# Kernel tuning notes

Measured on AMD Instinct MI355X. Metric: run time of the kernel, lower is better.

Reference implementation:

```python
import math
import jax, jax.numpy as jnp
import numpy as np
from jax import lax

# ---- static config (mirrors RPN init + typical torchvision anchor setup) ----
IMG_H = IMG_W = 800
LEVELS = [(200, 200, 4, 32), (100, 100, 8, 64), (50, 50, 16, 128), (25, 25, 32, 256), (13, 13, 64, 512)]  # (h, w, stride, anchor_size)
RATIOS = (0.5, 1.0, 2.0)
COUNTS = tuple(h * w * len(RATIOS) for (h, w, _, _) in LEVELS)  # (120000,30000,7500,1875,507)
A_TOTAL = sum(COUNTS)  # 159882
PRE_NMS = 2000
POST_NMS = 1000
NMS_THRESH = 0.7
MIN_SIZE = 1e-3
BBOX_CLIP = math.log(1000.0 / 16)


def make_anchors():
    parts = []
    for (h, w, stride, size) in LEVELS:
        ws = np.array([size * np.sqrt(1.0 / r) for r in RATIOS], np.float32)  # [3]
        hs = np.array([size * np.sqrt(r) for r in RATIOS], np.float32)
        sx = (np.arange(w, dtype=np.float32) + 0.5) * stride
        sy = (np.arange(h, dtype=np.float32) + 0.5) * stride
        cy, cx = np.meshgrid(sy, sx, indexing='ij')
        cx = cx.reshape(-1, 1)
        cy = cy.reshape(-1, 1)
        a = np.stack([cx - ws / 2, cy - hs / 2, cx + ws / 2, cy + hs / 2], axis=-1)  # [HW,3,4]
        parts.append(a.reshape(-1, 4))
    return np.concatenate(parts, 0).astype(np.float32)


def setup_inputs() -> dict:
    key = jax.random.key(0)
    k1, k2 = jax.random.split(key)
    scores = jax.random.normal(k1, (1, A_TOTAL), dtype=jnp.float32)
    deltas = jax.random.normal(k2, (A_TOTAL, 4), dtype=jnp.float32) * 0.5
    anchors = jnp.asarray(make_anchors())
    return {'scores': scores, 'deltas': deltas, 'anchors': anchors}


def _pairwise_iou(b):
    area = (b[:, 2] - b[:, 0]) * (b[:, 3] - b[:, 1])  # [K]
    lt = jnp.maximum(b[:, None, :2], b[None, :, :2])   # [K,K,2]
    rb = jnp.minimum(b[:, None, 2:], b[None, :, 2:])
    wh = jnp.maximum(rb - lt, 0.0)
    inter = wh[..., 0] * wh[..., 1]
    return inter / (area[:, None] + area[None, :] - inter)


def reference(scores, deltas, anchors):
    s_all = lax.stop_gradient(scores[0])  # original does cls.detach()
    # ---- box decode (torchvision-style) ----
    w = anchors[:, 2] - anchors[:, 0]
    h = anchors[:, 3] - anchors[:, 1]
    cx = anchors[:, 0] + 0.5 * w
    cy = anchors[:, 1] + 0.5 * h
    dx, dy = deltas[:, 0], deltas[:, 1]
    dw = jnp.minimum(deltas[:, 2], BBOX_CLIP)
    dh = jnp.minimum(deltas[:, 3], BBOX_CLIP)
    px = cx + dx * w
    py = cy + dy * h
    pw = jnp.exp(dw) * w
    ph = jnp.exp(dh) * h
    boxes = jnp.stack([px - 0.5 * pw, py - 0.5 * ph, px + 0.5 * pw, py + 0.5 * ph], axis=1)  # [A,4]
    # ---- per-level top-k over objectness ----
    idx_parts = []
    off = 0
    for c in COUNTS:
        k = min(PRE_NMS, c)
        _, ti = lax.top_k(lax.dynamic_slice_in_dim(s_all, off, c), k)
        idx_parts.append(ti + off)
        off += c
    top_idx = jnp.concatenate(idx_parts)  # [K=8382]
    K = top_idx.shape[0]
    s = s_all[top_idx]
    b = boxes[top_idx]
    # ---- clip to image + min-size validity (masked instead of compacted) ----
    b = jnp.stack([jnp.clip(b[:, 0], 0.0, IMG_W), jnp.clip(b[:, 1], 0.0, IMG_H),
                   jnp.clip(b[:, 2], 0.0, IMG_W), jnp.clip(b[:, 3], 0.0, IMG_H)], axis=1)
    valid = ((b[:, 2] - b[:, 0]) >= MIN_SIZE) & ((b[:, 3] - b[:, 1]) >= MIN_SIZE)
    # ---- per-level NMS offset; replicates original feature_mask[keep] indexing
    # (positional indexing into the full anchor-order level-id vector) ----
    fmask_full = np.concatenate([np.full(c, i, np.float32) for i, c in enumerate(COUNTS)])
    fmask = jnp.asarray(fmask_full[:K])
    box_max = jnp.max(jnp.where(valid[:, None], b, -jnp.inf))
    bn = b + (fmask * (box_max + 1.0))[:, None]
    # ---- greedy NMS on score-sorted candidates ----
    s_m = jnp.where(valid, s, -jnp.inf)
    order = jnp.argsort(-s_m)
    s_srt = s_m[order]
    b_srt = b[order]
    iou = _pairwise_iou(bn[order])  # [K,K] ~281MB
    ar = jnp.arange(K)

    def body(i, keep):
        sup = (iou[i] > NMS_THRESH) & (ar > i)
        return jnp.where(keep[i], keep & ~sup, keep)

    keep = lax.fori_loop(0, K, body, s_srt > -jnp.inf)
    final = jnp.where(keep, s_srt, -jnp.inf)
    out_s, oidx = lax.top_k(final, POST_NMS)  # top post_nms kept, score order; -inf pads
    out_b = b_srt[oidx]
    return out_b, out_s
```

## Files before the change

### kernel.cpp

```cpp
#include <hip/hip_runtime.h>
#include <math.h>

typedef unsigned int u32;
typedef unsigned long long u64;
typedef unsigned char u8;

#define K_TOT 8382
#define NCH 131
#define CAP 1024
#define EC 64
#define DC 8
#define GCAP 32768
#define IMGSZ 800.0f

__device__ __constant__ int LOFF[5] = {0, 120000, 150000, 157500, 159375};
__device__ __constant__ int LCNT[5] = {120000, 30000, 7500, 1875, 507};
__device__ __constant__ int KSEL[5] = {2000, 2000, 2000, 1875, 507};
__device__ __constant__ int SELB[5] = {0, 2000, 4000, 6000, 7875};
__device__ __constant__ int HBS[4] = {0, 118, 148, 156};
__device__ __constant__ int GBS[6] = {0, 118, 148, 156, 158, 159};

static __device__ __forceinline__ u32 fkey(float x) {
    u32 u = __float_as_uint(x);
    u32 m = (u32)(((int)u) >> 31) | 0x80000000u;
    return u ^ m;
}

static __device__ __forceinline__ int lvl_of(int s) {
    return (s < 2000) ? 0 : (s < 4000) ? 1 : (s < 6000) ? 2 : (s < 7875) ? 3 : 4;
}

static __device__ __forceinline__ u32 rdl32(u32 v, int j) {
    return (u32)__builtin_amdgcn_readlane((int)v, j);
}
static __device__ __forceinline__ u64 rdlane64(u64 v, int j) {
    u32 lo = (u32)__builtin_amdgcn_readlane((int)(u32)v, j);
    u32 hi = (u32)__builtin_amdgcn_readlane((int)(u32)(v >> 32), j);
    return ((u64)hi << 32) | (u64)lo;
}

static __device__ __forceinline__ void thresh_scan(const u32* hist, u32* scanbuf, int m,
                                                   u32 need, u32* sv, int t) {
    for (int i = t; i < m; i += 1024) scanbuf[i] = hist[m - 1 - i];
    __syncthreads();
    for (int ofs = 1; ofs < m; ofs <<= 1) {
        int i0 = t, i1 = t + 1024;
        u32 a0 = 0, a1 = 0;
        if (i0 < m && i0 >= ofs) a0 = scanbuf[i0 - ofs];
        if (i1 < m && i1 >= ofs) a1 = scanbuf[i1 - ofs];
        __syncthreads();
        if (i0 < m && i0 >= ofs) scanbuf[i0] += a0;
        if (i1 < m && i1 >= ofs) scanbuf[i1] += a1;
        __syncthreads();
    }
    for (int i = t; i < m; i += 1024) {
        u32 inc = scanbuf[i];
        u32 exc = i ? scanbuf[i - 1] : 0;
        if (inc >= need && exc < need) { sv[0] = (u32)(m - 1 - i); sv[1] = need - exc; }
    }
    __syncthreads();
}

__global__ __launch_bounds__(1024) void k_hist(const float* __restrict__ scores,
                                               u32* __restrict__ hist3) {
    __shared__ u32 lh[2048];
    int t = threadIdx.x;
    lh[t] = 0; lh[t + 1024] = 0;
    __syncthreads();
    int b = blockIdx.x;
    int l = (b < HBS[1]) ? 0 : (b < HBS[2]) ? 1 : 2;
    int i = (b - HBS[l]) * 1024 + t;
    if (i < LCNT[l]) atomicAdd(&lh[fkey(scores[LOFF[l] + i]) >> 21], 1u);
    __syncthreads();
    u32* h = hist3 + l * 2048;
    if (lh[t]) atomicAdd(&h[t], lh[t]);
    if (lh[t + 1024]) atomicAdd(&h[t + 1024], lh[t + 1024]);
}

__global__ __launch_bounds__(1024) void k_thresh(const u32* __restrict__ hist3,
                                                 u32* __restrict__ tinfo) {
    __shared__ u32 scanbuf[2048];
    __shared__ u32 sv[2];
    int l = blockIdx.x;
    int t = threadIdx.x;
    thresh_scan(hist3 + l * 2048, scanbuf, 2048, (u32)KSEL[l], sv, t);
    if (t == 0) { tinfo[l * 2] = sv[0]; tinfo[l * 2 + 1] = sv[1]; }
}

__global__ __launch_bounds__(1024) void k_gather(const float* __restrict__ scores,
                                                 const u32* __restrict__ tinfo,
                                                 u32* __restrict__ sel, u32* __restrict__ cgt,
                                                 u32* __restrict__ gcnt, u32* __restrict__ gidx,
                                                 u32* __restrict__ gkey) {
    int b = blockIdx.x;
    int l = (b < GBS[1]) ? 0 : (b < GBS[2]) ? 1 : (b < GBS[3]) ? 2 : (b < GBS[4]) ? 3 : 4;
    int i = (b - GBS[l]) * 1024 + threadIdx.x;
    if (i >= LCNT[l]) return;
    int off = LOFF[l], sb = SELB[l];
    if (l >= 3) { sel[sb + i] = (u32)(off + i); return; }
    u32 ky = fkey(scores[off + i]);
    u32 b1 = tinfo[l * 2];
    u32 top = ky >> 21;
    if (top > b1) {
        u32 p = atomicAdd(&cgt[l], 1u);
        sel[sb + p] = (u32)(off + i);
    } else if (top == b1) {
        u32 e = atomicAdd(&gcnt[l], 1u);
        if (e < GCAP) { gidx[l * GCAP + e] = (u32)i; gkey[l * GCAP + e] = ky; }
    }
}

__global__ __launch_bounds__(1024) void k_final(const u32* __restrict__ gidx,
                                                const u32* __restrict__ gkey,
                                                const u32* __restrict__ gcnt,
                                                const u32* __restrict__ tinfo,
                                                u32* __restrict__ sel) {
    __shared__ u32 hist[2048];
    __shared__ u32 scanbuf[2048];
    __shared__ u32 eqbuf[1024];
    __shared__ u32 sv[2];
    __shared__ u32 c2, ceq;
    int l = blockIdx.x;
    int t = threadIdx.x;
    int k = KSEL[l], sb = SELB[l], off = LOFF[l];
    u32 m = gcnt[l]; if (m > GCAP) m = GCAP;
    u32 b1 = tinfo[l * 2];
    u32 need = tinfo[l * 2 + 1];
    const u32* kb = gkey + l * GCAP;
    const u32* ib = gidx + l * GCAP;
    hist[t] = 0; hist[t + 1024] = 0; __syncthreads();
    for (u32 e = t; e < m; e += 1024) atomicAdd(&hist[(kb[e] >> 10) & 2047u], 1u);
    __syncthreads();
    thresh_scan(hist, scanbuf, 2048, need, sv, t);
    u32 b2 = sv[0], need2 = sv[1];
    __syncthreads();
    hist[t] = 0; __syncthreads();
    for (u32 e = t; e < m; e += 1024) {
        u32 ky = kb[e];
        if (((ky >> 10) & 2047u) == b2) atomicAdd(&hist[ky & 1023u], 1u);
    }
    __syncthreads();
    thresh_scan(hist, scanbuf, 1024, need2, sv, t);
    u32 T = (b1 << 21) | (b2 << 10) | sv[0];
    u32 take = sv[1];
    if (t == 0) { c2 = 0; ceq = 0; }
    __syncthreads();
    u32 nGTbin = need - take;
    u32 base2 = (u32)sb + (u32)k - need;
    for (u32 e = t; e < m; e += 1024) {
        u32 ky = kb[e];
        if (ky > T) { u32 p = atomicAdd(&c2, 1u); sel[base2 + p] = (u32)off + ib[e]; }
        else if (ky == T) { u32 q = atomicAdd(&ceq, 1u); if (q < 1024) eqbuf[q] = ib[e]; }
    }
    __syncthreads();
    if (t == 0) {
        int n = (ceq > 1024u) ? 1024 : (int)ceq;
        for (int a = 1; a < n; ++a) {
            u32 v = eqbuf[a]; int bq = a - 1;
            while (bq >= 0 && eqbuf[bq] > v) { eqbuf[bq + 1] = eqbuf[bq]; --bq; }
            eqbuf[bq + 1] = v;
        }
        for (u32 q = 0; q < take; ++q) sel[base2 + nGTbin + q] = (u32)off + eqbuf[q];
    }
}

__global__ void k_decode(const float* __restrict__ scores, const float4* __restrict__ deltas,
                         const float4* __restrict__ anchors, const u32* __restrict__ sel,
                         float4* __restrict__ candB, float* __restrict__ candS,
                         u32* __restrict__ candV, u32* __restrict__ candA) {
    int s = blockIdx.x * 256 + threadIdx.x;
    if (s >= K_TOT) return;
    u32 a = sel[s];
    float4 an = anchors[a];
    float4 dl = deltas[a];
    float sc = scores[a];
    float w = __fsub_rn(an.z, an.x), h = __fsub_rn(an.w, an.y);
    float cx = __fadd_rn(an.x, __fmul_rn(0.5f, w));
    float cy = __fadd_rn(an.y, __fmul_rn(0.5f, h));
    const float CLIPV = (float)4.1351665567423563;
    float dw = fminf(dl.z, CLIPV);
    float dh = fminf(dl.w, CLIPV);
    float px = __fadd_rn(cx, __fmul_rn(dl.x, w));
    float py = __fadd_rn(cy, __fmul_rn(dl.y, h));
    float pw = __fmul_rn((float)exp((double)dw), w);
    float ph = __fmul_rn((float)exp((double)dh), h);
    float x1 = __fsub_rn(px, __fmul_rn(0.5f, pw));
    float y1 = __fsub_rn(py, __fmul_rn(0.5f, ph));
    float x2 = __fadd_rn(px, __fmul_rn(0.5f, pw));
    float y2 = __fadd_rn(py, __fmul_rn(0.5f, ph));
    x1 = fminf(fmaxf(x1, 0.0f), IMGSZ);
    y1 = fminf(fmaxf(y1, 0.0f), IMGSZ);
    x2 = fminf(fmaxf(x2, 0.0f), IMGSZ);
    y2 = fminf(fmaxf(y2, 0.0f), IMGSZ);
    bool valid = (__fsub_rn(x2, x1) >= 0.001f) && (__fsub_rn(y2, y1) >= 0.001f);
    candB[s] = make_float4(x1, y1, x2, y2);
    candS[s] = sc;
    candV[s] = valid ? 1u : 0u;
    candA[s] = a;
}

__global__ __launch_bounds__(256) void k_rank_lvl(const float* __restrict__ candS,
                                                  const u32* __restrict__ candA,
                                                  u32* __restrict__ Praw) {
    __shared__ u64 tile[256];
    int l = blockIdx.z;
    int cnt = KSEL[l], base = SELB[l];
    int tx = blockIdx.x * 256;
    int ty = blockIdx.y * 256;
    if (tx >= cnt || ty >= cnt) return;
    int t = threadIdx.x;
    u64 Aj = ~0ull;
    if (tx + t < cnt) {
        int j = base + tx + t;
        Aj = ((u64)(~fkey(candS[j])) << 32) | (u64)candA[j];
    }
    tile[t] = Aj;
    __syncthreads();
    int si = ty + t;
    if (si >= cnt) return;
    int s = base + si;
    u64 A = ((u64)(~fkey(candS[s])) << 32) | (u64)candA[s];
    int r = 0;
#pragma unroll 8
    for (int q = 0; q < 256; ++q) r += (tile[q] < A);
    if (r) atomicAdd(&Praw[s], (u32)r);
}

__global__ __launch_bounds__(256) void k_rank_glob(const float* __restrict__ candS,
                                                   const u32* __restrict__ candV,
                                                   const u32* __restrict__ Praw,
                                                   u32* __restrict__ rank) {
    __shared__ u64 colB[256];
    int t = threadIdx.x;
    int cj = blockIdx.x * 256 + t;
    u64 B = ~0ull;
    if (cj < K_TOT) {
        u32 smk = candV[cj] ? fkey(candS[cj]) : 0x007FFFFFu;
        u32 Pj = (u32)SELB[lvl_of(cj)] + Praw[cj];
        B = ((u64)(~smk) << 32) | (u64)Pj;
    }
    colB[t] = B;
    __syncthreads();
    int s = blockIdx.y * 256 + t;
    if (s >= K_TOT) return;
    u32 smk = candV[s] ? fkey(candS[s]) : 0x007FFFFFu;
    u32 Ps = (u32)SELB[lvl_of(s)] + Praw[s];
    u64 myB = ((u64)(~smk) << 32) | (u64)Ps;
    int cnt = 0;
#pragma unroll 8
    for (int j = 0; j < 256; ++j) cnt += (colB[j] < myB);
    if (cnt) atomicAdd(&rank[s], (u32)cnt);
}

__global__ void k_scatter(const float4* __restrict__ candB, const float* __restrict__ candS,
                          const u32* __restrict__ candV, const u32* __restrict__ rank,
                          float4* __restrict__ sB, float* __restrict__ sArea,
                          float* __restrict__ sS, u64* __restrict__ vwords) {
    int s = blockIdx.x * 256 + threadIdx.x;
    if (s >= K_TOT) return;
    u32 r = rank[s];
    float4 b = candB[s];
    float area = __fmul_rn(__fsub_rn(b.z, b.x), __fsub_rn(b.w, b.y));
    sB[r] = b; sArea[r] = area; sS[r] = candS[s];
    if (candV[s]) atomicOr(&vwords[r >> 6], 1ull << (r & 63));
}

__global__ __launch_bounds__(256) void k_mask(const float4* __restrict__ sB,
                                              const float* __restrict__ sArea,
                                              u64* __restrict__ diag, u32* __restrict__ ecnt,
                                              ulonglong2* __restrict__ epack,
                                              u32* __restrict__ dcnt, u64* __restrict__ dmask,
                                              ulonglong2* __restrict__ dpack) {
    __shared__ float4 cb[64];
    __shared__ float ca[64];
    int wd = blockIdx.x;
    int t = threadIdx.x;
    if (t < 64) {
        int j = wd * 64 + t;
        if (j < K_TOT) { cb[t] = sB[j]; ca[t] = sArea[j]; }
        else { cb[t] = make_float4(0.f, 0.f, 0.f, 0.f); ca[t] = 0.f; }
    }
    __syncthreads();
    int i = blockIdx.y * 256 + t;
    if (i >= K_TOT) return;
    int dwr = i >> 6;
    if (wd < dwr) return;
    float4 bi = sB[i];
    float ai = sArea[i];
    u64 bits = 0;
    int jbase = wd * 64;
    for (int j2 = 0; j2 < 64; ++j2) {
        int j = jbase + j2;
        if (j > i && j < K_TOT) {
            float4 bj = cb[j2];
            float ltx = fmaxf(bi.x, bj.x), lty = fmaxf(bi.y, bj.y);
            float rbx = fminf(bi.z, bj.z), rby = fminf(bi.w, bj.w);
            float wx = fmaxf(__fsub_rn(rbx, ltx), 0.0f);
            float wy = fmaxf(__fsub_rn(rby, lty), 0.0f);
            float inter = __fmul_rn(wx, wy);
            if (inter > 0.0f) {
                float uni = __fsub_rn(__fadd_rn(ai, ca[j2]), inter);
                float iou = inter / uni;
                if (iou > 0.7f) bits |= (1ull << j2);
            }
        }
    }
    if (wd == dwr) {
        diag[i] = bits;
        if (bits != 0ull) {
            u32 p = atomicAdd(&dcnt[dwr], 1u);
            if (p < DC) dpack[dwr * DC + p] = make_ulonglong2((u64)(i & 63), bits);
            atomicOr(&dmask[dwr], 1ull << (i & 63));
        }
    } else if (bits != 0ull) {
        u32 p = atomicAdd(&ecnt[dwr], 1u);
        if (p < CAP) epack[dwr * CAP + p] = make_ulonglong2((u64)((i & 63) | (wd << 6)), bits);
    }
}

__global__ __launch_bounds__(64) void k_scan(const u64* __restrict__ diag,
                                             const u64* __restrict__ vwords,
                                             const u32* __restrict__ ecnt,
                                             const ulonglong2* __restrict__ epack,
                                             const u32* __restrict__ dcnt,
                                             const u64* __restrict__ dmask,
                                             const ulonglong2* __restrict__ dpack,
                                             u64* __restrict__ keepw) {
    __shared__ ulonglong2 sEpack[NCH * EC];
    __shared__ ulonglong2 sDpack[NCH * DC];
    volatile __shared__ u64 sR[NCH];
    __shared__ u64 sKeep[NCH];
    int lane = threadIdx.x;
    u64 v0, v1, v2, m0, m1, m2;
    u32 c0, c1, c2, d0, d1, d2;
    {
        int i0 = lane, i1 = lane + 64, i2 = lane + 128;
        bool p2 = (i2 < NCH);
        v0 = vwords[i0]; v1 = vwords[i1]; v2 = p2 ? vwords[i2] : 0;
        c0 = ecnt[i0]; c1 = ecnt[i1]; c2 = p2 ? ecnt[i2] : 0;
        d0 = dcnt[i0]; d1 = dcnt[i1]; d2 = p2 ? dcnt[i2] : 0;
        m0 = dmask[i0]; m1 = dmask[i1]; m2 = p2 ? dmask[i2] : 0;
        if (c0 > CAP) c0 = CAP;
        if (c1 > CAP) c1 = CAP;
        if (c2 > CAP) c2 = CAP;
        sR[i0] = 0; sR[i1] = 0;
        if (p2) sR[i2] = 0;
    }
    for (int base = 0; base < NCH; base += 16) {
        ulonglong2 tmp[16];
        int nb = NCH - base; if (nb > 16) nb = 16;
#pragma unroll
        for (int b = 0; b < 16; ++b)
            if (b < nb) tmp[b] = epack[(size_t)(base + b) * CAP + lane];
#pragma unroll
        for (int b = 0; b < 16; ++b)
            if (b < nb) sEpack[(base + b) * EC + lane] = tmp[b];
    }
    for (int base = 0; base < NCH * DC; base += 64 * 8) {
        ulonglong2 tmp[8];
#pragma unroll
        for (int b = 0; b < 8; ++b) {
            int i = base + b * 64 + lane;
            if (i < NCH * DC) tmp[b] = dpack[i];
        }
#pragma unroll
        for (int b = 0; b < 8; ++b) {
            int i = base + b * 64 + lane;
            if (i < NCH * DC) sDpack[i] = tmp[b];
        }
    }
    __syncthreads();
    u64 r_cur = 0;
    ulonglong2 E = sEpack[lane];
    ulonglong2 DP = (lane < DC) ? sDpack[lane] : make_ulonglong2(~0ull, 0ull);
    u32 cnt = rdl32(c0, 0), dn = rdl32(d0, 0);
    u64 vw = rdlane64(v0, 0), dmw = rdlane64(m0, 0);
    for (int c = 0; c < NCH; ++c) {
        int cn = (c + 1 < NCH) ? (c + 1) : c;
        u64 rpre = sR[cn];
        ulonglong2 En = sEpack[cn * EC + lane];
        ulonglong2 DPn = (lane < DC) ? sDpack[cn * DC + lane] : make_ulonglong2(~0ull, 0ull);
        u32 cntn, dnn; u64 vwn, dmn;
        if (cn < 64)       { cntn = rdl32(c0, cn);       dnn = rdl32(d0, cn);       vwn = rdlane64(v0, cn);       dmn = rdlane64(m0, cn); }
        else if (cn < 128) { cntn = rdl32(c1, cn - 64);  dnn = rdl32(d1, cn - 64);  vwn = rdlane64(v1, cn - 64);  dmn = rdlane64(m1, cn - 64); }
        else               { cntn = rdl32(c2, cn - 128); dnn = rdl32(d2, cn - 128); vwn = rdlane64(v2, cn - 128); dmn = rdlane64(m2, cn - 128); }

        u64 alive = vw & ~r_cur;
        if (dn) {
            if (dn <= (u32)DC) {
                u64 dm = dmw & alive;
                u32 ml = ((u32)lane < dn) ? (u32)DP.x : 0xFFu;
                while (dm) {
                    int j = __builtin_ctzll(dm);
                    dm &= dm - 1;
                    if ((alive >> j) & 1ull) {
                        u64 selm = __ballot(ml == (u32)j);
                        int src = __builtin_ctzll(selm);
                        alive &= ~rdlane64(DP.y, src);
                    }
                }
            } else {
                int r = c * 64 + lane;
                u64 D = (r < K_TOT) ? diag[r] : 0ull;
                u64 nzd = __ballot(D != 0ull);
                nzd &= alive;
                while (nzd) {
                    int j = __builtin_ctzll(nzd);
                    nzd &= nzd - 1;
                    if ((alive >> j) & 1ull) alive &= ~rdlane64(D, j);
                }
            }
        }
        if (lane == 0) sKeep[c] = alive;
        u32 tc = (u32)E.x >> 6;
        bool act = ((u32)lane < cnt) && (((alive >> ((u32)E.x & 63u)) & 1ull) != 0ull);
        if (act) atomicOr((u64*)&sR[tc], E.y);
        bool redo = false;
        if (cnt > (u32)EC) {
            for (u32 e = (u32)EC + (u32)lane; e < cnt; e += 64u) {
                ulonglong2 Et = epack[(size_t)c * CAP + e];
                u32 pk = (u32)Et.x;
                if ((alive >> (pk & 63u)) & 1ull) atomicOr((u64*)&sR[pk >> 6], Et.y);
            }
            redo = true;
        }
        u64 selm = __ballot(act && (tc == (u32)cn));
        u64 contrib = 0;
        while (selm) {
            int j = __builtin_ctzll(selm);
            selm &= selm - 1;
            contrib |= rdlane64(E.y, j);
        }
        if (redo) rpre = sR[cn];
        r_cur = rpre | contrib;
        E = En; DP = DPn; cnt = cntn; dn = dnn; vw = vwn; dmw = dmn;
    }
    __syncthreads();
    for (int i = lane; i < NCH; i += 64) keepw[i] = sKeep[i];
}

__global__ __launch_bounds__(1024) void k_out(const u64* __restrict__ keepw,
                                              const float4* __restrict__ sB,
                                              const float* __restrict__ sS,
                                              float* __restrict__ out) {
    __shared__ u64 skw[NCH];
    __shared__ u32 pc[NCH + 1];
    int t = threadIdx.x;
    if (t < NCH) {
        u64 kw = keepw[t];
        skw[t] = kw;
        pc[t + 1] = (u32)__popcll(kw);
    }
    if (t == 0) pc[0] = 0;
    __syncthreads();
    for (int ofs = 1; ofs < NCH; ofs <<= 1) {
        int i = t + 1;
        u32 v = 0;
        bool p = (t < NCH) && (i - ofs >= 1);
        if (p) v = pc[i - ofs];
        __syncthreads();
        if (p) pc[i] += v;
        __syncthreads();
    }
    u32 nk = pc[NCH];
    for (int i = t; i < K_TOT; i += 1024) {
        int w = i >> 6, b = i & 63;
        u64 kw = skw[w];
        u32 kb = pc[w] + (u32)__popcll(kw & ((1ull << b) - 1ull));
        bool kp = (kw >> b) & 1ull;
        if (kp) {
            if (kb < 1000u) {
                float4 bx = sB[i];
                out[kb * 4 + 0] = bx.x; out[kb * 4 + 1] = bx.y;
                out[kb * 4 + 2] = bx.z; out[kb * 4 + 3] = bx.w;
                out[4000 + kb] = sS[i];
            }
        } else {
            u32 q = (u32)i - kb;
            u32 slot = nk + q;
            if (slot < 1000u) {
                float4 bx = sB[i];
                out[slot * 4 + 0] = bx.x; out[slot * 4 + 1] = bx.y;
                out[slot * 4 + 2] = bx.z; out[slot * 4 + 3] = bx.w;
                out[4000 + slot] = -INFINITY;
            }
        }
    }
}

static constexpr size_t al256(size_t x) { return (x + 255) & ~(size_t)255; }
static constexpr size_t KB4 = (size_t)K_TOT * 4;
static constexpr size_t KB16 = (size_t)K_TOT * 16;
static constexpr size_t O_RANK = 0;
static constexpr size_t O_PRAW = al256(O_RANK + KB4);
static constexpr size_t O_ECNT = al256(O_PRAW + KB4);
static constexpr size_t O_DCNT = al256(O_ECNT + (size_t)NCH * 4);
static constexpr size_t O_DMASK = al256(O_DCNT + (size_t)NCH * 4);
static constexpr size_t O_VW = al256(O_DMASK + (size_t)NCH * 8);
static constexpr size_t O_HIST = al256(O_VW + (size_t)NCH * 8);
static constexpr size_t O_CGT = al256(O_HIST + (size_t)3 * 2048 * 4);
static constexpr size_t O_GCNT = al256(O_CGT + 3 * 4);
static constexpr size_t MEMSET_BYTES = al256(O_GCNT + 3 * 4);
static constexpr size_t O_TINFO = MEMSET_BYTES;
static constexpr size_t O_SEL = al256(O_TINFO + 6 * 4);
static constexpr size_t O_GIDX = al256(O_SEL + KB4);
static constexpr size_t O_GKEY = al256(O_GIDX + (size_t)3 * GCAP * 4);
static constexpr size_t O_CANDB = al256(O_GKEY + (size_t)3 * GCAP * 4);
static constexpr size_t O_CANDS = al256(O_CANDB + KB16);
static constexpr size_t O_CANDV = al256(O_CANDS + KB4);
static constexpr size_t O_CANDA = al256(O_CANDV + KB4);
static constexpr size_t O_SB = al256(O_CANDA + KB4);
static constexpr size_t O_SAREA = al256(O_SB + KB16);
static constexpr size_t O_SS = al256(O_SAREA + KB4);
static constexpr size_t O_KW = al256(O_SS + KB4);
static constexpr size_t O_DIAG = al256(O_KW + (size_t)NCH * 8);
static constexpr size_t O_EPACK = al256(O_DIAG + (size_t)(NCH * 64) * 8);
static constexpr size_t O_DPACK = al256(O_EPACK + (size_t)NCH * CAP * 16);

extern "C" void kernel_launch(void* const* d_in, const int* in_sizes, int n_in,
                              void* d_out, int out_size, void* d_ws, size_t ws_size,
                              hipStream_t stream) {
    const float* scores = (const float*)d_in[0];
    const float4* deltas = (const float4*)d_in[1];
    const float4* anchors = (const float4*)d_in[2];
    float* out = (float*)d_out;
    char* ws = (char*)d_ws;

    u32* rank = (u32*)(ws + O_RANK);
    u32* Praw = (u32*)(ws + O_PRAW);
    u32* ecnt = (u32*)(ws + O_ECNT);
    u32* dcnt = (u32*)(ws + O_DCNT);
    u64* dmask = (u64*)(ws + O_DMASK);
    u64* vwords = (u64*)(ws + O_VW);
    u32* hist3 = (u32*)(ws + O_HIST);
    u32* cgt = (u32*)(ws + O_CGT);
    u32* gcnt = (u32*)(ws + O_GCNT);
    u32* tinfo = (u32*)(ws + O_TINFO);
    u32* sel = (u32*)(ws + O_SEL);
    u32* gidx = (u32*)(ws + O_GIDX);
    u32* gkey = (u32*)(ws + O_GKEY);
    float4* candB = (float4*)(ws + O_CANDB);
    float* candS = (float*)(ws + O_CANDS);
    u32* candV = (u32*)(ws + O_CANDV);
    u32* candA = (u32*)(ws + O_CANDA);
    float4* sB = (float4*)(ws + O_SB);
    float* sArea = (float*)(ws + O_SAREA);
    float* sS = (float*)(ws + O_SS);
    u64* keepw = (u64*)(ws + O_KW);
    u64* diag = (u64*)(ws + O_DIAG);
    ulonglong2* epack = (ulonglong2*)(ws + O_EPACK);
    ulonglong2* dpack = (ulonglong2*)(ws + O_DPACK);

    hipMemsetAsync(ws, 0, MEMSET_BYTES, stream);

    const int NBLK = (K_TOT + 255) / 256;
    k_hist<<<156, 1024, 0, stream>>>(scores, hist3);
    k_thresh<<<3, 1024, 0, stream>>>(hist3, tinfo);
    k_gather<<<159, 1024, 0, stream>>>(scores, tinfo, sel, cgt, gcnt, gidx, gkey);
    k_final<<<3, 1024, 0, stream>>>(gidx, gkey, gcnt, tinfo, sel);
    k_decode<<<NBLK, 256, 0, stream>>>(scores, deltas, anchors, sel, candB, candS, candV, candA);
    k_rank_lvl<<<dim3(8, 8, 5), 256, 0, stream>>>(candS, candA, Praw);
    k_rank_glob<<<dim3(NBLK, NBLK), 256, 0, stream>>>(candS, candV, Praw, rank);
    k_scatter<<<NBLK, 256, 0, stream>>>(candB, candS, candV, rank, sB, sArea, sS, vwords);
    k_mask<<<dim3(NCH, NBLK), 256, 0, stream>>>(sB, sArea, diag, ecnt, epack, dcnt, dmask, dpack);
    k_scan<<<1, 64, 0, stream>>>(diag, vwords, ecnt, epack, dcnt, dmask, dpack, keepw);
    k_out<<<1, 1024, 0, stream>>>(keepw, sB, sS, out);
}
```

Measured before the change: 228.1 us.

## Switch NMS scan to pull-based suppression and fuse output into scan kernel

Cross-chunk suppression entries are now bucketed by target chunk instead of source chunk. The scan pulls each source's keep bit from per-lane keep registers using ds_bpermute and reduces with DPP OR, replacing the shared-memory atomicOr push. The valid-word bitmap is now built with a ballot in k_mask rather than global atomics in k_scatter. k_out is folded into a 1024-thread k_scan, which removes one launch and the keepw round trip. The trade-off is a heavier serial per-chunk pull-and-reduce path, and the shared-memory load is now spread over 16 waves.

```diff
diff --git a/kernel.cpp b/kernel.cpp
--- a/kernel.cpp
+++ b/kernel.cpp
@@ -37,6 +37,29 @@
     u32 lo = (u32)__builtin_amdgcn_readlane((int)(u32)v, j);
     u32 hi = (u32)__builtin_amdgcn_readlane((int)(u32)(v >> 32), j);
     return ((u64)hi << 32) | (u64)lo;
+}
+
+static __device__ __forceinline__ u32 wor32(u32 x) {
+    x |= (u32)__builtin_amdgcn_update_dpp(0, (int)x, 0x111, 0xf, 0xf, true);
+    x |= (u32)__builtin_amdgcn_update_dpp(0, (int)x, 0x112, 0xf, 0xf, true);
+    x |= (u32)__builtin_amdgcn_update_dpp(0, (int)x, 0x114, 0xf, 0xf, true);
+    x |= (u32)__builtin_amdgcn_update_dpp(0, (int)x, 0x118, 0xf, 0xf, true);
+    x |= (u32)__builtin_amdgcn_update_dpp(0, (int)x, 0x142, 0xa, 0xf, true);
+    x |= (u32)__builtin_amdgcn_update_dpp(0, (int)x, 0x143, 0xc, 0xf, true);
+    return x;
+}
+
+static __device__ __forceinline__ u64 pullkeep(u64 k0, u64 k1, u64 k2, u32 sch) {
+    int bidx = (int)((sch & 63u) << 2);
+    u32 a0l = (u32)__builtin_amdgcn_ds_bpermute(bidx, (int)(u32)k0);
+    u32 a0h = (u32)__builtin_amdgcn_ds_bpermute(bidx, (int)(u32)(k0 >> 32));
+    u32 a1l = (u32)__builtin_amdgcn_ds_bpermute(bidx, (int)(u32)k1);
+    u32 a1h = (u32)__builtin_amdgcn_ds_bpermute(bidx, (int)(u32)(k1 >> 32));
+    u32 a2l = (u32)__builtin_amdgcn_ds_bpermute(bidx, (int)(u32)k2);
+    u32 a2h = (u32)__builtin_amdgcn_ds_bpermute(bidx, (int)(u32)(k2 >> 32));
+    return (sch < 64) ? (((u64)a0h << 32) | (u64)a0l)
+         : (sch < 128) ? (((u64)a1h << 32) | (u64)a1l)
+                       : (((u64)a2h << 32) | (u64)a2l);
 }
 
 static __device__ __forceinline__ void thresh_scan(const u32* hist, u32* scanbuf, int m,
@@ -255,18 +278,19 @@
 __global__ void k_scatter(const float4* __restrict__ candB, const float* __restrict__ candS,
                           const u32* __restrict__ candV, const u32* __restrict__ rank,
                           float4* __restrict__ sB, float* __restrict__ sArea,
-                          float* __restrict__ sS, u64* __restrict__ vwords) {
+                          float* __restrict__ sS, u32* __restrict__ sV) {
     int s = blockIdx.x * 256 + threadIdx.x;
     if (s >= K_TOT) return;
     u32 r = rank[s];
     float4 b = candB[s];
     float area = __fmul_rn(__fsub_rn(b.z, b.x), __fsub_rn(b.w, b.y));
-    sB[r] = b; sArea[r] = area; sS[r] = candS[s];
-    if (candV[s]) atomicOr(&vwords[r >> 6], 1ull << (r & 63));
+    sB[r] = b; sArea[r] = area; sS[r] = candS[s]; sV[r] = candV[s];
 }
 
 __global__ __launch_bounds__(256) void k_mask(const float4* __restrict__ sB,
                                               const float* __restrict__ sArea,
+                                              const u32* __restrict__ sV,
+                                              u64* __restrict__ vwords,
                                               u64* __restrict__ diag, u32* __restrict__ ecnt,
                                               ulonglong2* __restrict__ epack,
                                               u32* __restrict__ dcnt, u64* __restrict__ dmask,
@@ -307,33 +331,53 @@
     }
     if (wd == dwr) {
         diag[i] = bits;
+        u64 vb = __ballot(sV[i] != 0u);
+        if ((i & 63) == 0) vwords[wd] = vb;
         if (bits != 0ull) {
             u32 p = atomicAdd(&dcnt[dwr], 1u);
             if (p < DC) dpack[dwr * DC + p] = make_ulonglong2((u64)(i & 63), bits);
             atomicOr(&dmask[dwr], 1ull << (i & 63));
         }
     } else if (bits != 0ull) {
-        u32 p = atomicAdd(&ecnt[dwr], 1u);
-        if (p < CAP) epack[dwr * CAP + p] = make_ulonglong2((u64)((i & 63) | (wd << 6)), bits);
-    }
-}
-
-__global__ __launch_bounds__(64) void k_scan(const u64* __restrict__ diag,
-                                             const u64* __restrict__ vwords,
-                                             const u32* __restrict__ ecnt,
-                                             const ulonglong2* __restrict__ epack,
-                                             const u32* __restrict__ dcnt,
-                                             const u64* __restrict__ dmask,
-                                             const ulonglong2* __restrict__ dpack,
-                                             u64* __restrict__ keepw) {
-    __shared__ ulonglong2 sEpack[NCH * EC];
+        u32 p = atomicAdd(&ecnt[wd], 1u);
+        if (p < CAP) epack[wd * CAP + p] = make_ulonglong2((u64)i, bits);
+    }
+}
+
+__global__ __launch_bounds__(1024) void k_scan(const u64* __restrict__ diag,
+                                               const u64* __restrict__ vwords,
+                                               const u32* __restrict__ ecnt,
+                                               const ulonglong2* __restrict__ tpack,
+                                               const u32* __restrict__ dcnt,
+                                               const u64* __restrict__ dmask,
+                                               const ulonglong2* __restrict__ dpack,
+                                               const float4* __restrict__ sB,
+                                               const float* __restrict__ sS,
+                                               float* __restrict__ out) {
+    __shared__ ulonglong2 sTpack[NCH * EC];
     __shared__ ulonglong2 sDpack[NCH * DC];
-    volatile __shared__ u64 sR[NCH];
     __shared__ u64 sKeep[NCH];
-    int lane = threadIdx.x;
-    u64 v0, v1, v2, m0, m1, m2;
-    u32 c0, c1, c2, d0, d1, d2;
+    __shared__ u32 pc[NCH + 1];
+    int t = threadIdx.x;
+    int w = t >> 6, lane = t & 63;
     {
+        ulonglong2 tmp[9];
+        int nb = 0;
+        for (int ch = w; ch < NCH; ch += 16) tmp[nb++] = tpack[(size_t)ch * CAP + lane];
+        nb = 0;
+        for (int ch = w; ch < NCH; ch += 16) sTpack[ch * EC + lane] = tmp[nb++];
+    }
+    {
+        ulonglong2 a0, a1;
+        bool p0 = t < NCH * DC, p1 = (t + 1024) < NCH * DC;
+        if (p0) a0 = dpack[t];
+        if (p1) a1 = dpack[t + 1024];
+        if (p0) sDpack[t] = a0;
+        if (p1) sDpack[t + 1024] = a1;
+    }
+    u64 v0 = 0, v1 = 0, v2 = 0, m0 = 0, m1 = 0, m2 = 0;
+    u32 c0 = 0, c1 = 0, c2 = 0, d0 = 0, d1 = 0, d2 = 0;
+    if (w == 0) {
         int i0 = lane, i1 = lane + 64, i2 = lane + 128;
         bool p2 = (i2 < NCH);
         v0 = vwords[i0]; v1 = vwords[i1]; v2 = p2 ? vwords[i2] : 0;
@@ -343,114 +387,77 @@
         if (c0 > CAP) c0 = CAP;
         if (c1 > CAP) c1 = CAP;
         if (c2 > CAP) c2 = CAP;
-        sR[i0] = 0; sR[i1] = 0;
-        if (p2) sR[i2] = 0;
-    }
-    for (int base = 0; base < NCH; base += 16) {
-        ulonglong2 tmp[16];
-        int nb = NCH - base; if (nb > 16) nb = 16;
-#pragma unroll
-        for (int b = 0; b < 16; ++b)
-            if (b < nb) tmp[b] = epack[(size_t)(base + b) * CAP + lane];
-#pragma unroll
-        for (int b = 0; b < 16; ++b)
-            if (b < nb) sEpack[(base + b) * EC + lane] = tmp[b];
-    }
-    for (int base = 0; base < NCH * DC; base += 64 * 8) {
-        ulonglong2 tmp[8];
-#pragma unroll
-        for (int b = 0; b < 8; ++b) {
-            int i = base + b * 64 + lane;
-            if (i < NCH * DC) tmp[b] = dpack[i];
-        }
-#pragma unroll
-        for (int b = 0; b < 8; ++b) {
-            int i = base + b * 64 + lane;
-            if (i < NCH * DC) sDpack[i] = tmp[b];
-        }
-    }
-    __syncthreads();
-    u64 r_cur = 0;
-    ulonglong2 E = sEpack[lane];
-    ulonglong2 DP = (lane < DC) ? sDpack[lane] : make_ulonglong2(~0ull, 0ull);
-    u32 cnt = rdl32(c0, 0), dn = rdl32(d0, 0);
-    u64 vw = rdlane64(v0, 0), dmw = rdlane64(m0, 0);
-    for (int c = 0; c < NCH; ++c) {
-        int cn = (c + 1 < NCH) ? (c + 1) : c;
-        u64 rpre = sR[cn];
-        ulonglong2 En = sEpack[cn * EC + lane];
-        ulonglong2 DPn = (lane < DC) ? sDpack[cn * DC + lane] : make_ulonglong2(~0ull, 0ull);
-        u32 cntn, dnn; u64 vwn, dmn;
-        if (cn < 64)       { cntn = rdl32(c0, cn);       dnn = rdl32(d0, cn);       vwn = rdlane64(v0, cn);       dmn = rdlane64(m0, cn); }
-        else if (cn < 128) { cntn = rdl32(c1, cn - 64);  dnn = rdl32(d1, cn - 64);  vwn = rdlane64(v1, cn - 64);  dmn = rdlane64(m1, cn - 64); }
-        else               { cntn = rdl32(c2, cn - 128); dnn = rdl32(d2, cn - 128); vwn = rdlane64(v2, cn - 128); dmn = rdlane64(m2, cn - 128); }
-
-        u64 alive = vw & ~r_cur;
-        if (dn) {
-            if (dn <= (u32)DC) {
-                u64 dm = dmw & alive;
-                u32 ml = ((u32)lane < dn) ? (u32)DP.x : 0xFFu;
-                while (dm) {
-                    int j = __builtin_ctzll(dm);
-                    dm &= dm - 1;
-                    if ((alive >> j) & 1ull) {
-                        u64 selm = __ballot(ml == (u32)j);
-                        int src = __builtin_ctzll(selm);
-                        alive &= ~rdlane64(DP.y, src);
+    }
+    __syncthreads();
+    if (w == 0) {
+        u64 k0 = 0, k1 = 0, k2 = 0;
+        ulonglong2 E = sTpack[lane];
+        ulonglong2 DP = (lane < DC) ? sDpack[lane] : make_ulonglong2(~0ull, 0ull);
+        u32 cnt = rdl32(c0, 0), dn = rdl32(d0, 0);
+        u64 vw = rdlane64(v0, 0), dmw = rdlane64(m0, 0);
+        for (int c = 0; c < NCH; ++c) {
+            int cn = (c + 1 < NCH) ? (c + 1) : c;
+            ulonglong2 En = sTpack[cn * EC + lane];
+            ulonglong2 DPn = (lane < DC) ? sDpack[cn * DC + lane] : make_ulonglong2(~0ull, 0ull);
+            u32 cntn, dnn; u64 vwn, dmn;
+            if (cn < 64)       { cntn = rdl32(c0, cn);       dnn = rdl32(d0, cn);       vwn = rdlane64(v0, cn);       dmn = rdlane64(m0, cn); }
+            else if (cn < 128) { cntn = rdl32(c1, cn - 64);  dnn = rdl32(d1, cn - 64);  vwn = rdlane64(v1, cn - 64);  dmn = rdlane64(m1, cn - 64); }
+            else               { cntn = rdl32(c2, cn - 128); dnn = rdl32(d2, cn - 128); vwn = rdlane64(v2, cn - 128); dmn = rdlane64(m2, cn - 128); }
+            u64 incoming = 0;
+            if (cnt) {
+                u64 mbits = 0;
+                {
+                    u32 sidx = (u32)E.x & 0x3FFFu;
+                    u64 kw = pullkeep(k0, k1, k2, sidx >> 6);
+                    if (((u32)lane < cnt) && ((kw >> (sidx & 63u)) & 1ull)) mbits = E.y;
+                }
+                if (cnt > (u32)EC) {
+                    for (u32 e = (u32)EC + (u32)lane; e < cnt; e += 64u) {
+                        ulonglong2 Et = tpack[(size_t)c * CAP + e];
+                        u32 sidx = (u32)Et.x & 0x3FFFu;
+                        u64 kw = pullkeep(k0, k1, k2, sidx >> 6);
+                        if ((kw >> (sidx & 63u)) & 1ull) mbits |= Et.y;
                     }
                 }
-            } else {
-                int r = c * 64 + lane;
-                u64 D = (r < K_TOT) ? diag[r] : 0ull;
-                u64 nzd = __ballot(D != 0ull);
-                nzd &= alive;
-                while (nzd) {
-                    int j = __builtin_ctzll(nzd);
-                    nzd &= nzd - 1;
-                    if ((alive >> j) & 1ull) alive &= ~rdlane64(D, j);
+                u32 lo = wor32((u32)mbits);
+                u32 hi = wor32((u32)(mbits >> 32));
+                incoming = ((u64)rdl32(hi, 63) << 32) | (u64)rdl32(lo, 63);
+            }
+            u64 alive = vw & ~incoming;
+            if (dn) {
+                if (dn <= (u32)DC) {
+                    u64 dm = dmw & alive;
+                    u32 ml = ((u32)lane < dn) ? (u32)DP.x : 0xFFu;
+                    while (dm) {
+                        int j = __builtin_ctzll(dm);
+                        dm &= dm - 1;
+                        if ((alive >> j) & 1ull) {
+                            u64 selm = __ballot(ml == (u32)j);
+                            int src = __builtin_ctzll(selm);
+                            alive &= ~rdlane64(DP.y, src);
+                        }
+                    }
+                } else {
+                    int r = c * 64 + lane;
+                    u64 D = (r < K_TOT) ? diag[r] : 0ull;
+                    u64 nzd = __ballot(D != 0ull);
+                    nzd &= alive;
+                    while (nzd) {
+                        int j = __builtin_ctzll(nzd);
+                        nzd &= nzd - 1;
+                        if ((alive >> j) & 1ull) alive &= ~rdlane64(D, j);
+                    }
                 }
             }
+            if (lane == 0) sKeep[c] = alive;
+            if (c < 64)       { if (lane == c)       k0 = alive; }
+            else if (c < 128) { if (lane == c - 64)  k1 = alive; }
+            else              { if (lane == c - 128) k2 = alive; }
+            E = En; DP = DPn; cnt = cntn; dn = dnn; vw = vwn; dmw = dmn;
         }
-        if (lane == 0) sKeep[c] = alive;
-        u32 tc = (u32)E.x >> 6;
-        bool act = ((u32)lane < cnt) && (((alive >> ((u32)E.x & 63u)) & 1ull) != 0ull);
-        if (act) atomicOr((u64*)&sR[tc], E.y);
-        bool redo = false;
-        if (cnt > (u32)EC) {
-            for (u32 e = (u32)EC + (u32)lane; e < cnt; e += 64u) {
-                ulonglong2 Et = epack[(size_t)c * CAP + e];
-                u32 pk = (u32)Et.x;
-                if ((alive >> (pk & 63u)) & 1ull) atomicOr((u64*)&sR[pk >> 6], Et.y);
-            }
-            redo = true;
-        }
-        u64 selm = __ballot(act && (tc == (u32)cn));
-        u64 contrib = 0;
-        while (selm) {
-            int j = __builtin_ctzll(selm);
-            selm &= selm - 1;
-            contrib |= rdlane64(E.y, j);
-        }
-        if (redo) rpre = sR[cn];
-        r_cur = rpre | contrib;
-        E = En; DP = DPn; cnt = cntn; dn = dnn; vw = vwn; dmw = dmn;
-    }
-    __syncthreads();
-    for (int i = lane; i < NCH; i += 64) keepw[i] = sKeep[i];
-}
-
-__global__ __launch_bounds__(1024) void k_out(const u64* __restrict__ keepw,
-                                              const float4* __restrict__ sB,
-                                              const float* __restrict__ sS,
-                                              float* __restrict__ out) {
-    __shared__ u64 skw[NCH];
-    __shared__ u32 pc[NCH + 1];
-    int t = threadIdx.x;
-    if (t < NCH) {
-        u64 kw = keepw[t];
-        skw[t] = kw;
-        pc[t + 1] = (u32)__popcll(kw);
-    }
+    }
+    __syncthreads();
+    if (t < NCH) pc[t + 1] = (u32)__popcll(sKeep[t]);
     if (t == 0) pc[0] = 0;
     __syncthreads();
     for (int ofs = 1; ofs < NCH; ofs <<= 1) {
@@ -464,9 +471,9 @@
     }
     u32 nk = pc[NCH];
     for (int i = t; i < K_TOT; i += 1024) {
-        int w = i >> 6, b = i & 63;
-        u64 kw = skw[w];
-        u32 kb = pc[w] + (u32)__popcll(kw & ((1ull << b) - 1ull));
+        int wi = i >> 6, b = i & 63;
+        u64 kw = sKeep[wi];
+        u32 kb = pc[wi] + (u32)__popcll(kw & ((1ull << b) - 1ull));
         bool kp = (kw >> b) & 1ull;
         if (kp) {
             if (kb < 1000u) {
@@ -496,8 +503,7 @@
 static constexpr size_t O_ECNT = al256(O_PRAW + KB4);
 static constexpr size_t O_DCNT = al256(O_ECNT + (size_t)NCH * 4);
 static constexpr size_t O_DMASK = al256(O_DCNT + (size_t)NCH * 4);
-static constexpr size_t O_VW = al256(O_DMASK + (size_t)NCH * 8);
-static constexpr size_t O_HIST = al256(O_VW + (size_t)NCH * 8);
+static constexpr size_t O_HIST = al256(O_DMASK + (size_t)NCH * 8);
 static constexpr size_t O_CGT = al256(O_HIST + (size_t)3 * 2048 * 4);
 static constexpr size_t O_GCNT = al256(O_CGT + 3 * 4);
 static constexpr size_t MEMSET_BYTES = al256(O_GCNT + 3 * 4);
@@ -512,8 +518,9 @@
 static constexpr size_t O_SB = al256(O_CANDA + KB4);
 static constexpr size_t O_SAREA = al256(O_SB + KB16);
 static constexpr size_t O_SS = al256(O_SAREA + KB4);
-static constexpr size_t O_KW = al256(O_SS + KB4);
-static constexpr size_t O_DIAG = al256(O_KW + (size_t)NCH * 8);
+static constexpr size_t O_SV = al256(O_SS + KB4);
+static constexpr size_t O_VW = al256(O_SV + KB4);
+static constexpr size_t O_DIAG = al256(O_VW + (size_t)NCH * 8);
 static constexpr size_t O_EPACK = al256(O_DIAG + (size_t)(NCH * 64) * 8);
 static constexpr size_t O_DPACK = al256(O_EPACK + (size_t)NCH * CAP * 16);
 
@@ -531,7 +538,6 @@
     u32* ecnt = (u32*)(ws + O_ECNT);
     u32* dcnt = (u32*)(ws + O_DCNT);
     u64* dmask = (u64*)(ws + O_DMASK);
-    u64* vwords = (u64*)(ws + O_VW);
     u32* hist3 = (u32*)(ws + O_HIST);
     u32* cgt = (u32*)(ws + O_CGT);
     u32* gcnt = (u32*)(ws + O_GCNT);
@@ -546,7 +552,8 @@
     float4* sB = (float4*)(ws + O_SB);
     float* sArea = (float*)(ws + O_SAREA);
     float* sS = (float*)(ws + O_SS);
-    u64* keepw = (u64*)(ws + O_KW);
+    u32* sV = (u32*)(ws + O_SV);
+    u64* vwords = (u64*)(ws + O_VW);
     u64* diag = (u64*)(ws + O_DIAG);
     ulonglong2* epack = (ulonglong2*)(ws + O_EPACK);
     ulonglong2* dpack = (ulonglong2*)(ws + O_DPACK);
@@ -561,8 +568,7 @@
     k_decode<<<NBLK, 256, 0, stream>>>(scores, deltas, anchors, sel, candB, candS, candV, candA);
     k_rank_lvl<<<dim3(8, 8, 5), 256, 0, stream>>>(candS, candA, Praw);
     k_rank_glob<<<dim3(NBLK, NBLK), 256, 0, stream>>>(candS, candV, Praw, rank);
-    k_scatter<<<NBLK, 256, 0, stream>>>(candB, candS, candV, rank, sB, sArea, sS, vwords);
-    k_mask<<<dim3(NCH, NBLK), 256, 0, stream>>>(sB, sArea, diag, ecnt, epack, dcnt, dmask, dpack);
-    k_scan<<<1, 64, 0, stream>>>(diag, vwords, ecnt, epack, dcnt, dmask, dpack, keepw);
-    k_out<<<1, 1024, 0, stream>>>(keepw, sB, sS, out);
-}
+    k_scatter<<<NBLK, 256, 0, stream>>>(candB, candS, candV, rank, sB, sArea, sS, sV);
+    k_mask<<<dim3(NCH, NBLK), 256, 0, stream>>>(sB, sArea, sV, vwords, diag, ecnt, epack, dcnt, dmask, dpack);
+    k_scan<<<1, 1024, 0, stream>>>(diag, vwords, ecnt, epack, dcnt, dmask, dpack, sB, sS, out);
+}
```

New measurement: 220.6 us. -3.3%, faster.
